# Kernel tuning notes

Hardware: AMD Instinct MI355X
Metric: run time of the kernel (lower is better)

The kernel has to match this reference:

```python
import jax, jax.numpy as jnp
import numpy as np

DELTA = 128  # bell patch size (self.delta)
S2P = np.sqrt(2 * np.pi)


def _gauss(r, sigma=1.0):
    a = 1.0
    return np.exp(-(((r - a) / (2 * sigma)) ** 2)) / S2P


def _bell_5gauss(r):
    out = np.zeros_like(r)
    for s in range(5):
        sigma = 2 * s + 1
        out += 2 / 5 * np.pi * sigma ** 2 * _gauss(r, sigma)
    return out


def _make_bell():
    # r = distance from patch center (DELTA/2, DELTA/2)
    x = np.arange(DELTA)[:, None]
    y = np.arange(DELTA)[None, :]
    r = np.sqrt((x - DELTA / 2) ** 2 + (y - DELTA / 2) ** 2)
    return jnp.asarray(_bell_5gauss(r), dtype=jnp.float32)


def setup_inputs() -> dict:
    key = jax.random.key(0)
    k1, k2 = jax.random.split(key)
    B, L, H, W = 16, 68, 224, 224
    pred_heatmap = jax.random.normal(k1, (B, L, H, W), dtype=jnp.float32)
    # landmarks are (y, x) pixel coordinates within the image
    true_landmarks = jax.random.uniform(k2, (B, L, 2), dtype=jnp.float32) * 223.0
    bell = _make_bell()
    return {"pred_heatmap": pred_heatmap, "true_landmarks": true_landmarks, "bell": bell}


def reference(pred_heatmap, true_landmarks, bell):
    B, L, H, W = pred_heatmap.shape
    half = DELTA // 2
    yx = jnp.round(true_landmarks).astype(jnp.int32)  # [B, L, 2], order (y, x)
    y_r = yx[..., 0]
    x_r = yx[..., 1]
    # bell row index for image row i: i - x_r + half; valid iff in [0, DELTA)
    bx = jnp.arange(H, dtype=jnp.int32)[None, None, :] - x_r[..., None] + half  # [B,L,H]
    by = jnp.arange(W, dtype=jnp.int32)[None, None, :] - y_r[..., None] + half  # [B,L,W]
    vx = (bx >= 0) & (bx < DELTA)
    vy = (by >= 0) & (by < DELTA)
    bxc = jnp.clip(bx, 0, DELTA - 1)
    byc = jnp.clip(by, 0, DELTA - 1)
    # gather the clipped-window patch into the full [B,L,H,W] target heatmap
    true_heatmap = bell[bxc[..., :, None], byc[..., None, :]]
    mask = (vx[..., :, None] & vy[..., None, :]).astype(pred_heatmap.dtype)
    true_heatmap = true_heatmap * mask
    diff = pred_heatmap - true_heatmap
    return jnp.mean(diff * diff)
```

## Files before the change

### kernel.cpp

```cpp
#include <hip/hip_runtime.h>

#define N_IMG   1088
#define IMG_HW  50176
#define W_DIM   224
#define H_DIM   224
#define ROW_F4  56
#define IMG_F4  12544
#define DELTA_  128
#define HALF_   64
#define N_TOT   54591488.0

__global__ __launch_bounds__(256) void lm_loss_partial(
        const float* __restrict__ pred,
        const float* __restrict__ lms,
        const float* __restrict__ bell,
        float* __restrict__ partials) {
    const int img = blockIdx.x;
    const float4* __restrict__ p4 =
        (const float4*)(pred + (size_t)img * IMG_HW);

    const float ly = lms[img * 2 + 0];
    const float lx = lms[img * 2 + 1];
    const int y_r = (int)rintf(ly);
    const int x_r = (int)rintf(lx);

    float acc = 0.0f;
    for (int f = threadIdx.x; f < IMG_F4; f += 256) {
        const int h  = f / ROW_F4;
        const int w  = (f - h * ROW_F4) * 4;
        const float4 p = p4[f];

        float t0 = 0.f, t1 = 0.f, t2 = 0.f, t3 = 0.f;
        const int bx = h - x_r + HALF_;
        if ((unsigned)bx < (unsigned)DELTA_) {
            const float* __restrict__ row = bell + bx * DELTA_;
            const int by = w - y_r + HALF_;
            if ((unsigned)(by + 0) < (unsigned)DELTA_) t0 = row[by + 0];
            if ((unsigned)(by + 1) < (unsigned)DELTA_) t1 = row[by + 1];
            if ((unsigned)(by + 2) < (unsigned)DELTA_) t2 = row[by + 2];
            if ((unsigned)(by + 3) < (unsigned)DELTA_) t3 = row[by + 3];
        }
        const float d0 = p.x - t0;
        const float d1 = p.y - t1;
        const float d2 = p.z - t2;
        const float d3 = p.w - t3;
        acc += d0 * d0;
        acc += d1 * d1;
        acc += d2 * d2;
        acc += d3 * d3;
    }

    #pragma unroll
    for (int off = 32; off > 0; off >>= 1)
        acc += __shfl_down(acc, off, 64);

    __shared__ float wsum[4];
    const int lane = threadIdx.x & 63;
    const int wid  = threadIdx.x >> 6;
    if (lane == 0) wsum[wid] = acc;
    __syncthreads();
    if (threadIdx.x == 0)
        partials[img] = wsum[0] + wsum[1] + wsum[2] + wsum[3];
}

__global__ __launch_bounds__(256) void lm_loss_final(
        const float* __restrict__ partials,
        float* __restrict__ out) {
    double acc = 0.0;
    for (int i = threadIdx.x; i < N_IMG; i += 256)
        acc += (double)partials[i];

    #pragma unroll
    for (int off = 32; off > 0; off >>= 1)
        acc += __shfl_down(acc, off, 64);

    __shared__ double wsum[4];
    const int lane = threadIdx.x & 63;
    const int wid  = threadIdx.x >> 6;
    if (lane == 0) wsum[wid] = acc;
    __syncthreads();
    if (threadIdx.x == 0) {
        const double total = wsum[0] + wsum[1] + wsum[2] + wsum[3];
        out[0] = (float)(total / N_TOT);
    }
}

extern "C" void kernel_launch(void* const* d_in, const int* in_sizes, int n_in,
                              void* d_out, int out_size, void* d_ws, size_t ws_size,
                              hipStream_t stream) {
    const float* pred = (const float*)d_in[0];
    const float* lms  = (const float*)d_in[1];
    const float* bell = (const float*)d_in[2];
    float* out        = (float*)d_out;
    float* partials   = (float*)d_ws;

    lm_loss_partial<<<N_IMG, 256, 0, stream>>>(pred, lms, bell, partials);
    lm_loss_final<<<1, 256, 0, stream>>>(partials, out);
}
```

Measured before the change: 304.4 us.

## Split each image across seven blocks and make bell lookups branchless

Each image is now processed by seven blocks, each covering a fixed slice of 1792 float4 elements, in a fully unrolled loop of seven iterations. The aim is more blocks in flight and more independent loads per thread to hide HBM latency. Bell lookups now use clamped indices and are always issued, then masked with selects instead of branches, which removes divergence but adds cached loads outside the patch. The final reduction sums seven times as many partials.

```diff
diff --git a/kernel.cpp b/kernel.cpp
--- a/kernel.cpp
+++ b/kernel.cpp
@@ -1,45 +1,52 @@
 #include <hip/hip_runtime.h>
 
-#define N_IMG   1088
-#define IMG_HW  50176
-#define W_DIM   224
-#define H_DIM   224
-#define ROW_F4  56
-#define IMG_F4  12544
-#define DELTA_  128
-#define HALF_   64
-#define N_TOT   54591488.0
+#define N_IMG    1088
+#define IMG_HW   50176
+#define ROW_F4   56
+#define IMG_F4   12544
+#define SLICES   7
+#define SLICE_F4 1792
+#define N_PART   (N_IMG * SLICES)
+#define N_TOT    54591488.0
 
 __global__ __launch_bounds__(256) void lm_loss_partial(
         const float* __restrict__ pred,
         const float* __restrict__ lms,
         const float* __restrict__ bell,
         float* __restrict__ partials) {
-    const int img = blockIdx.x;
+    const int img   = blockIdx.x;
+    const int slice = blockIdx.y;
     const float4* __restrict__ p4 =
         (const float4*)(pred + (size_t)img * IMG_HW);
 
-    const float ly = lms[img * 2 + 0];
-    const float lx = lms[img * 2 + 1];
-    const int y_r = (int)rintf(ly);
-    const int x_r = (int)rintf(lx);
+    const int y_r = (int)rintf(lms[img * 2 + 0]);
+    const int x_r = (int)rintf(lms[img * 2 + 1]);
+    const int base = slice * SLICE_F4;
 
     float acc = 0.0f;
-    for (int f = threadIdx.x; f < IMG_F4; f += 256) {
+    #pragma unroll
+    for (int i = 0; i < 7; ++i) {
+        const int f = base + i * 256 + (int)threadIdx.x;
+        const float4 p = p4[f];
+
         const int h  = f / ROW_F4;
         const int w  = (f - h * ROW_F4) * 4;
-        const float4 p = p4[f];
+        const int bx = h - x_r + 64;
+        const int by = w - y_r + 64;
 
-        float t0 = 0.f, t1 = 0.f, t2 = 0.f, t3 = 0.f;
-        const int bx = h - x_r + HALF_;
-        if ((unsigned)bx < (unsigned)DELTA_) {
-            const float* __restrict__ row = bell + bx * DELTA_;
-            const int by = w - y_r + HALF_;
-            if ((unsigned)(by + 0) < (unsigned)DELTA_) t0 = row[by + 0];
-            if ((unsigned)(by + 1) < (unsigned)DELTA_) t1 = row[by + 1];
-            if ((unsigned)(by + 2) < (unsigned)DELTA_) t2 = row[by + 2];
-            if ((unsigned)(by + 3) < (unsigned)DELTA_) t3 = row[by + 3];
-        }
+        const int bxc = min(max(bx, 0), 127);
+        const float* __restrict__ row = bell + (bxc << 7);
+        const bool rowok = ((unsigned)bx < 128u);
+
+        float t0 = row[min(max(by + 0, 0), 127)];
+        float t1 = row[min(max(by + 1, 0), 127)];
+        float t2 = row[min(max(by + 2, 0), 127)];
+        float t3 = row[min(max(by + 3, 0), 127)];
+        t0 = (rowok && (unsigned)(by + 0) < 128u) ? t0 : 0.0f;
+        t1 = (rowok && (unsigned)(by + 1) < 128u) ? t1 : 0.0f;
+        t2 = (rowok && (unsigned)(by + 2) < 128u) ? t2 : 0.0f;
+        t3 = (rowok && (unsigned)(by + 3) < 128u) ? t3 : 0.0f;
+
         const float d0 = p.x - t0;
         const float d1 = p.y - t1;
         const float d2 = p.z - t2;
@@ -60,14 +67,14 @@
     if (lane == 0) wsum[wid] = acc;
     __syncthreads();
     if (threadIdx.x == 0)
-        partials[img] = wsum[0] + wsum[1] + wsum[2] + wsum[3];
+        partials[slice * N_IMG + img] = wsum[0] + wsum[1] + wsum[2] + wsum[3];
 }
 
 __global__ __launch_bounds__(256) void lm_loss_final(
         const float* __restrict__ partials,
         float* __restrict__ out) {
     double acc = 0.0;
-    for (int i = threadIdx.x; i < N_IMG; i += 256)
+    for (int i = threadIdx.x; i < N_PART; i += 256)
         acc += (double)partials[i];
 
     #pragma unroll
@@ -94,6 +101,7 @@
     float* out        = (float*)d_out;
     float* partials   = (float*)d_ws;
 
-    lm_loss_partial<<<N_IMG, 256, 0, stream>>>(pred, lms, bell, partials);
+    dim3 grid(N_IMG, SLICES);
+    lm_loss_partial<<<grid, 256, 0, stream>>>(pred, lms, bell, partials);
     lm_loss_final<<<1, 256, 0, stream>>>(partials, out);
 }
```

New measurement: 307.8 us. Within noise of the previous version (+1.1%).
